# Optimization experiments

Hardware: AMD Instinct MI355X
Metric: run time of the kernel (lower is better)

Reference implementation:

```python
import jax, jax.numpy as jnp
import numpy as np

N_NODES = 10000
N_EDGES = 640000
D = 128
BN_EPS = 1e-5


def setup_inputs() -> dict:
    key = jax.random.key(0)
    k1, k2, k3 = jax.random.split(key, 3)
    x = jax.random.normal(k1, (N_NODES, D), dtype=jnp.float32)
    edge_index = jax.random.randint(k2, (2, N_EDGES), 0, N_NODES, dtype=jnp.int64)
    W = jax.random.normal(k3, (D, D), dtype=jnp.float32) * (1.0 / np.sqrt(D))
    b = jnp.zeros((D,), dtype=jnp.float32)
    gamma = jnp.ones((D,), dtype=jnp.float32)
    beta = jnp.zeros((D,), dtype=jnp.float32)
    return {"x": x, "edge_index": edge_index, "W": W, "b": b, "gamma": gamma, "beta": beta}


def reference(x, edge_index, W, b, gamma, beta):
    # GINConv: out_i = MLP((1+eps)*x_i + sum_{j->i} x_j), eps=0
    src = edge_index[0]
    dst = edge_index[1]
    agg = jax.ops.segment_sum(x[src], dst, num_segments=N_NODES)  # [N, D]
    h = agg + x  # (1 + eps) * x with eps = 0
    # MLP inside GINConv: Linear + ReLU
    h = jnp.maximum(h @ W + b, 0.0)
    # outer F.relu (idempotent after inner ReLU, kept for faithfulness)
    h = jnp.maximum(h, 0.0)
    # BatchNorm1d, training-mode batch statistics (biased variance)
    mean = jnp.mean(h, axis=0)
    var = jnp.var(h, axis=0)
    h = (h - mean) * jax.lax.rsqrt(var + BN_EPS) * gamma + beta
    # Dropout in eval mode -> identity. his_x = [h]; return the main output.
    return h
```

## Files before the change

kernel.cpp:

```cpp
#include <hip/hip_runtime.h>

#define N_NODES 10000
#define N_EDGES 640000
#define D 128
#define BN_EPS 1e-5f
#define CAP 128
#define NSTRIPE 16
#define RPB 8
#define SENT 10200
#define NSLICE 320
#define ESLICE 2000

typedef _Float16 half4_t __attribute__((ext_vector_type(4)));

__global__ __launch_bounds__(256) void k_build(
    const int* __restrict__ ei,
    const float4* __restrict__ x4,
    int* deg, int* __restrict__ ssrc,
    half4_t* __restrict__ xh)
{
    const int b = blockIdx.x;
    const int t = threadIdx.x;

    const int gtid = b * 256 + t;
    if (gtid < N_NODES * D / 4) {
        const float4 v = x4[gtid];
        half4_t h;
        h.x = (_Float16)v.x; h.y = (_Float16)v.y;
        h.z = (_Float16)v.z; h.w = (_Float16)v.w;
        xh[gtid] = h;
    }

    const unsigned base = (unsigned)deg[SENT];
    const int g     = b & 7;
    const int e0    = (b >> 3) * ESLICE;
    for (int idx = t; idx < ESLICE; idx += 256) {
        const int e = e0 + idx;
        const int d = ei[N_EDGES + e];
        if ((d & 7) == g) {
            const int s = ei[e];
            const unsigned pos = (unsigned)atomicAdd(&deg[d], 1) - base;
            if (pos < CAP) ssrc[(d << 7) + (int)pos] = s;
        }
    }
}

__global__ __launch_bounds__(256) void k_gmlp(
    const float* __restrict__ x,
    const half4_t* __restrict__ xh4,
    const int* __restrict__ deg,
    const int* __restrict__ ssrc,
    const float* __restrict__ W,
    const float* __restrict__ bias,
    float* __restrict__ out,
    float* __restrict__ stats)
{
    __shared__ float hs[RPB][D];
    const int tid  = threadIdx.x;
    const int wv   = tid >> 6;
    const int lane = tid & 63;
    const int h    = lane >> 5;
    const int l    = lane & 31;
    const unsigned dbase = (unsigned)deg[SENT];
    const float4* __restrict__ x4 = (const float4*)x;

    #pragma unroll
    for (int j = 0; j < 2; j++) {
        const int lrow = wv * 2 + j;
        const int node = blockIdx.x * RPB + lrow;
        unsigned n = (unsigned)deg[node] - dbase;
        if (n > CAP) n = CAP;
        const int off = node << 7;
        float4 acc = make_float4(0.f, 0.f, 0.f, 0.f);
        int i = 0;
        for (; i + 64 <= (int)n; i += 64) {
            const int sj = ssrc[off + i + lane];
            #pragma unroll
            for (int b = 0; b < 2; b++) {
                half4_t v[16];
                #pragma unroll
                for (int u = 0; u < 16; u++) {
                    const int p = b * 16 + u;
                    const int s = __shfl(sj, 2 * p + h, 64);
                    v[u] = xh4[(size_t)s * 32 + l];
                }
                #pragma unroll
                for (int u = 0; u < 16; u++) {
                    acc.x += (float)v[u].x; acc.y += (float)v[u].y;
                    acc.z += (float)v[u].z; acc.w += (float)v[u].w;
                }
            }
        }
        const int c = (int)n - i;
        if (c > 0) {
            const int sj = (lane < c) ? ssrc[off + i + lane] : 0;
            const int pairs = c >> 1;
            for (int t2 = 0; t2 < pairs; t2 += 16) {
                half4_t v[16];
                #pragma unroll
                for (int u = 0; u < 16; u++) {
                    const int s = __shfl(sj, (2 * (t2 + u) + h) & 63, 64);
                    v[u] = xh4[(size_t)s * 32 + l];
                }
                #pragma unroll
                for (int u = 0; u < 16; u++) {
                    if (t2 + u < pairs) {
                        acc.x += (float)v[u].x; acc.y += (float)v[u].y;
                        acc.z += (float)v[u].z; acc.w += (float)v[u].w;
                    }
                }
            }
            if (c & 1) {
                const int s = __shfl(sj, c - 1, 64);
                const half4_t vv = xh4[(size_t)s * 32 + l];
                if (h == 0) {
                    acc.x += (float)vv.x; acc.y += (float)vv.y;
                    acc.z += (float)vv.z; acc.w += (float)vv.w;
                }
            }
        }
        acc.x += __shfl_xor(acc.x, 32, 64);
        acc.y += __shfl_xor(acc.y, 32, 64);
        acc.z += __shfl_xor(acc.z, 32, 64);
        acc.w += __shfl_xor(acc.w, 32, 64);
        if (h == 0) {
            const float4 xv = x4[(size_t)node * 32 + l];
            float4 o;
            o.x = acc.x + xv.x; o.y = acc.y + xv.y;
            o.z = acc.z + xv.z; o.w = acc.w + xv.w;
            *(float4*)&hs[lrow][4 * l] = o;
        }
    }
    __syncthreads();

    const int col = tid & 127;
    const int rg  = tid >> 7;
    float a[4] = {0.f, 0.f, 0.f, 0.f};
    #pragma unroll 8
    for (int k = 0; k < D; k++) {
        const float w = W[k * D + col];
        #pragma unroll
        for (int r = 0; r < 4; r++)
            a[r] = fmaf(hs[rg * 4 + r][k], w, a[r]);
    }

    const float bcol = bias[col];
    float s1 = 0.f, s2 = 0.f;
    #pragma unroll
    for (int r = 0; r < 4; r++) {
        const float v = fmaxf(a[r] + bcol, 0.f);
        out[(size_t)(blockIdx.x * RPB + rg * 4 + r) * D + col] = v;
        s1 += v;
        s2 += v * v;
    }

    __syncthreads();
    float* red = &hs[0][0];
    red[tid]       = s1;
    red[256 + tid] = s2;
    __syncthreads();
    if (tid < D) {
        float* sp = &stats[(size_t)(blockIdx.x & (NSTRIPE - 1)) * 256];
        atomicAdd(&sp[tid],     red[tid]       + red[tid + 128]);
        atomicAdd(&sp[D + tid], red[256 + tid] + red[256 + tid + 128]);
    }
}

__global__ __launch_bounds__(256) void k_bn(
    float* out,
    const float* __restrict__ stats,
    const float* __restrict__ gamma,
    const float* __restrict__ beta)
{
    __shared__ float sc[D], sh[D];
    const int tid = threadIdx.x;
    if (tid < D) {
        const float fbase = stats[NSTRIPE * 256];
        float s = 0.f, q = 0.f;
        #pragma unroll
        for (int cp = 0; cp < NSTRIPE; cp++) {
            s += stats[cp * 256 + tid]     - fbase;
            q += stats[cp * 256 + D + tid] - fbase;
        }
        const float mean = s * (1.0f / N_NODES);
        const float var  = q * (1.0f / N_NODES) - mean * mean;
        const float scale = gamma[tid] * rsqrtf(var + BN_EPS);
        sc[tid] = scale;
        sh[tid] = beta[tid] - mean * scale;
    }
    __syncthreads();

    float4* o4 = (float4*)out;
    #pragma unroll
    for (int j = 0; j < 2; j++) {
        const int f = blockIdx.x * 512 + j * 256 + tid;
        const int c = (f & 31) << 2;
        float4 v = o4[f];
        v.x = v.x * sc[c]     + sh[c];
        v.y = v.y * sc[c + 1] + sh[c + 1];
        v.z = v.z * sc[c + 2] + sh[c + 2];
        v.w = v.w * sc[c + 3] + sh[c + 3];
        o4[f] = v;
    }
}

extern "C" void kernel_launch(void* const* d_in, const int* in_sizes, int n_in,
                              void* d_out, int out_size, void* d_ws, size_t ws_size,
                              hipStream_t stream)
{
    const float* x     = (const float*)d_in[0];
    const int*   ei    = (const int*)d_in[1];
    const float* W     = (const float*)d_in[2];
    const float* bias  = (const float*)d_in[3];
    const float* gamma = (const float*)d_in[4];
    const float* beta  = (const float*)d_in[5];
    float* out = (float*)d_out;

    int*     deg   = (int*)d_ws;
    float*   stats = (float*)(deg + 10240);
    int*     ssrc  = (int*)(stats + NSTRIPE * 256 + 8);
    half4_t* xh    = (half4_t*)(ssrc + (size_t)N_NODES * CAP);

    k_build<<<NSLICE * 8, 256, 0, stream>>>(ei, (const float4*)x, deg, ssrc, xh);
    k_gmlp<<<N_NODES / RPB, 256, 0, stream>>>(x, xh, deg, ssrc, W, bias, out, stats);
    k_bn<<<N_NODES * D / 2048, 256, 0, stream>>>(out, stats, gamma, beta);
}
```

Baseline: 140.6 us.

## Replace per-node global atomic CSR build with two-pass binned bucket sort

Edge bucketing becomes two passes. The first pass counts edges per 32-node bin in shared memory, reserves space with one global atomic per bin and writes packed (src, local dst) records. The second pass scatters each bin's records into per-node lists in shared memory and copies them out as 16-bit source indices along with exact degrees. This is meant to remove the many global atomics and scattered writes of the old per-edge build, and to halve the index bandwidth in the gather. It adds a kernel launch and an extra pass over the records, and it relies on the bin capacity (2400) holding for random input.

Measured after the change: 125.5 us. 10.8% less time.

```diff
diff --git a/kernel.cpp b/kernel.cpp
--- a/kernel.cpp
+++ b/kernel.cpp
@@ -7,49 +7,102 @@
 #define CAP 128
 #define NSTRIPE 16
 #define RPB 8
-#define SENT 10200
-#define NSLICE 320
-#define ESLICE 2000
+#define NB 313
+#define BCAP 2400
+#define ABLK 128
+#define ASLICE 5000
+#define CSENT 319
 
 typedef _Float16 half4_t __attribute__((ext_vector_type(4)));
-
-__global__ __launch_bounds__(256) void k_build(
+typedef unsigned short u16;
+
+__global__ __launch_bounds__(256) void k_bin(
     const int* __restrict__ ei,
     const float4* __restrict__ x4,
-    int* deg, int* __restrict__ ssrc,
+    int* cur,
+    int* __restrict__ recs,
     half4_t* __restrict__ xh)
 {
-    const int b = blockIdx.x;
-    const int t = threadIdx.x;
-
-    const int gtid = b * 256 + t;
-    if (gtid < N_NODES * D / 4) {
-        const float4 v = x4[gtid];
-        half4_t h;
-        h.x = (_Float16)v.x; h.y = (_Float16)v.y;
-        h.z = (_Float16)v.z; h.w = (_Float16)v.w;
-        xh[gtid] = h;
-    }
-
-    const unsigned base = (unsigned)deg[SENT];
-    const int g     = b & 7;
-    const int e0    = (b >> 3) * ESLICE;
-    for (int idx = t; idx < ESLICE; idx += 256) {
-        const int e = e0 + idx;
+    __shared__ int cnt[NB];
+    __shared__ int base[NB];
+    const int b = blockIdx.x, t = threadIdx.x;
+
+    {
+        const int n4 = N_NODES * D / 4;
+        for (int i = b * 256 + t; i < n4; i += ABLK * 256) {
+            const float4 v = x4[i];
+            half4_t h;
+            h.x = (_Float16)v.x; h.y = (_Float16)v.y;
+            h.z = (_Float16)v.z; h.w = (_Float16)v.w;
+            xh[i] = h;
+        }
+    }
+
+    for (int i = t; i < NB; i += 256) cnt[i] = 0;
+    __syncthreads();
+
+    const int e0 = b * ASLICE;
+    for (int i = t; i < ASLICE; i += 256)
+        atomicAdd(&cnt[ei[N_EDGES + e0 + i] >> 5], 1);
+    __syncthreads();
+
+    const unsigned cbase = (unsigned)cur[CSENT];
+    for (int i = t; i < NB; i += 256) {
+        const int c = cnt[i];
+        base[i] = (int)((unsigned)atomicAdd(&cur[i], c) - cbase);
+        cnt[i] = 0;
+    }
+    __syncthreads();
+
+    for (int i = t; i < ASLICE; i += 256) {
+        const int e = e0 + i;
         const int d = ei[N_EDGES + e];
-        if ((d & 7) == g) {
-            const int s = ei[e];
-            const unsigned pos = (unsigned)atomicAdd(&deg[d], 1) - base;
-            if (pos < CAP) ssrc[(d << 7) + (int)pos] = s;
-        }
-    }
+        const int s = ei[e];
+        const int bin = d >> 5;
+        const int p = base[bin] + atomicAdd(&cnt[bin], 1);
+        if (p < BCAP) recs[bin * BCAP + p] = (s << 5) | (d & 31);
+    }
+}
+
+__global__ __launch_bounds__(256) void k_fill(
+    const int* __restrict__ recs,
+    const int* __restrict__ cur,
+    int* __restrict__ deg,
+    u16* __restrict__ ssrc)
+{
+    __shared__ u16 lst[32 * CAP];
+    __shared__ int cnt[32];
+    const int bin = blockIdx.x, t = threadIdx.x;
+    if (t < 32) cnt[t] = 0;
+    __syncthreads();
+
+    const unsigned cbase = (unsigned)cur[CSENT];
+    int nrec = (int)((unsigned)cur[bin] - cbase);
+    if (nrec > BCAP) nrec = BCAP;
+
+    for (int i = t; i < nrec; i += 256) {
+        const int r = recs[bin * BCAP + i];
+        const int dl = r & 31;
+        const int p = atomicAdd(&cnt[dl], 1);
+        if (p < CAP) lst[dl * CAP + p] = (u16)(r >> 5);
+    }
+    __syncthreads();
+
+    const int maxn = N_NODES - bin * 32;
+    if (t < 32 && t < maxn)
+        deg[bin * 32 + t] = min(cnt[t], CAP);
+
+    const int4* s4 = (const int4*)lst;
+    int4* d4 = (int4*)(ssrc + (size_t)bin * 32 * CAP);
+    const int nch = (maxn >= 32) ? 512 : (maxn * CAP) / 8;
+    for (int i = t; i < nch; i += 256) d4[i] = s4[i];
 }
 
 __global__ __launch_bounds__(256) void k_gmlp(
     const float* __restrict__ x,
     const half4_t* __restrict__ xh4,
     const int* __restrict__ deg,
-    const int* __restrict__ ssrc,
+    const u16* __restrict__ ssrc,
     const float* __restrict__ W,
     const float* __restrict__ bias,
     float* __restrict__ out,
@@ -61,20 +114,18 @@
     const int lane = tid & 63;
     const int h    = lane >> 5;
     const int l    = lane & 31;
-    const unsigned dbase = (unsigned)deg[SENT];
     const float4* __restrict__ x4 = (const float4*)x;
 
     #pragma unroll
     for (int j = 0; j < 2; j++) {
         const int lrow = wv * 2 + j;
         const int node = blockIdx.x * RPB + lrow;
-        unsigned n = (unsigned)deg[node] - dbase;
-        if (n > CAP) n = CAP;
+        const int n = deg[node];
         const int off = node << 7;
         float4 acc = make_float4(0.f, 0.f, 0.f, 0.f);
         int i = 0;
-        for (; i + 64 <= (int)n; i += 64) {
-            const int sj = ssrc[off + i + lane];
+        for (; i + 64 <= n; i += 64) {
+            const int sj = (int)ssrc[off + i + lane];
             #pragma unroll
             for (int b = 0; b < 2; b++) {
                 half4_t v[16];
@@ -91,9 +142,9 @@
                 }
             }
         }
-        const int c = (int)n - i;
+        const int c = n - i;
         if (c > 0) {
-            const int sj = (lane < c) ? ssrc[off + i + lane] : 0;
+            const int sj = (lane < c) ? (int)ssrc[off + i + lane] : 0;
             const int pairs = c >> 1;
             for (int t2 = 0; t2 < pairs; t2 += 16) {
                 half4_t v[16];
@@ -218,10 +269,13 @@
 
     int*     deg   = (int*)d_ws;
     float*   stats = (float*)(deg + 10240);
-    int*     ssrc  = (int*)(stats + NSTRIPE * 256 + 8);
+    int*     cur   = (int*)(stats + NSTRIPE * 256 + 8);
+    int*     recs  = cur + 320;
+    u16*     ssrc  = (u16*)(recs + NB * BCAP);
     half4_t* xh    = (half4_t*)(ssrc + (size_t)N_NODES * CAP);
 
-    k_build<<<NSLICE * 8, 256, 0, stream>>>(ei, (const float4*)x, deg, ssrc, xh);
+    k_bin<<<ABLK, 256, 0, stream>>>(ei, (const float4*)x, cur, recs, xh);
+    k_fill<<<NB, 256, 0, stream>>>(recs, cur, deg, ssrc);
     k_gmlp<<<N_NODES / RPB, 256, 0, stream>>>(x, xh, deg, ssrc, W, bias, out, stats);
     k_bn<<<N_NODES * D / 2048, 256, 0, stream>>>(out, stats, gamma, beta);
 }
```
